# Kernel optimization log

Measured on AMD Instinct MI355X. Metric: run time of the kernel, lower is better.

Reference implementation:

```python
import jax, jax.numpy as jnp
import numpy as np

NUM_HEADS = 16
KEY_SIZE = 64
HEAD_SIZE = 64


def setup_inputs() -> dict:
    key = jax.random.key(0)
    ks = jax.random.split(key, 8)
    B, S, D = 2, 2048, 1024
    s = 1.0 / np.sqrt(D)
    return {
        "q": jax.random.normal(ks[0], (B, S, D), jnp.float32),
        "k": jax.random.normal(ks[1], (B, S, D), jnp.float32),
        "v": jax.random.normal(ks[2], (B, S, D), jnp.float32),
        "v_mask": jax.random.randint(ks[3], (B, S), 0, 2, jnp.int32),
        "Wq": jax.random.normal(ks[4], (D, NUM_HEADS * KEY_SIZE), jnp.float32) * s,
        "Wk": jax.random.normal(ks[5], (D, NUM_HEADS * KEY_SIZE), jnp.float32) * s,
        "Wv": jax.random.normal(ks[6], (D, NUM_HEADS * HEAD_SIZE), jnp.float32) * s,
    }


def reference(q, k, v, v_mask, Wq, Wk, Wv):
    B, Sq, _ = q.shape
    Sk = k.shape[1]
    # projections + split heads: [B, S, H, d]
    qw = (q @ Wq).reshape(B, Sq, NUM_HEADS, KEY_SIZE)
    kw = (k @ Wk).reshape(B, Sk, NUM_HEADS, KEY_SIZE)
    vw = (v @ Wv).reshape(B, Sk, NUM_HEADS, HEAD_SIZE)
    # scores [B, H, Sq, Sk]
    a = jnp.einsum('bqhd,bkhd->bhqk', qw, kw) / np.sqrt(KEY_SIZE).astype(np.float32)
    # additive mask over key axis: x*m - (1-m)*1e12
    m = v_mask.astype(a.dtype)[:, None, None, :]
    a = a * m - (1.0 - m) * 1e12
    a = jax.nn.softmax(a, axis=-1)
    # output [B, Sq, H*head_size]
    o = jnp.einsum('bhqk,bkhd->bqhd', a, vw)
    return o.reshape(B, Sq, NUM_HEADS * HEAD_SIZE)
```

## Files before the change

### kernel.cpp

```cpp
#include <hip/hip_runtime.h>
#include <hip/hip_bf16.h>


#define SEQ 2048
#define DIM 1024
#define NPROJ 1024

typedef __bf16 bf16x8 __attribute__((ext_vector_type(8)));
typedef float floatx4 __attribute__((ext_vector_type(4)));
typedef float floatx16 __attribute__((ext_vector_type(16)));

__device__ inline unsigned short f2bf_bits(float x) {
  __hip_bfloat16 h = __float2bfloat16(x);
  return __builtin_bit_cast(unsigned short, h);
}

__device__ __forceinline__ void gload_lds16(const void* g, void* l) {
  __builtin_amdgcn_global_load_lds((const __attribute__((address_space(1))) void*)g,
                                   (__attribute__((address_space(3))) void*)l, 16, 0, 0);
}

__global__ __launch_bounds__(256) void cvt_x(
    const float* __restrict__ q, const float* __restrict__ k, const float* __restrict__ v,
    unsigned short* __restrict__ xb)
{
  const float* X = blockIdx.z == 0 ? q : (blockIdx.z == 1 ? k : v);
  unsigned short* O = xb + (size_t)blockIdx.z * 4096 * 1024;
  int i0 = blockIdx.x * 256 + threadIdx.x;
  #pragma unroll
  for (int it = 0; it < 4; ++it) {
    int i = i0 + it * 262144;
    float4 f = *reinterpret_cast<const float4*>(&X[(size_t)i * 4]);
    ushort4 o;
    o.x = f2bf_bits(f.x); o.y = f2bf_bits(f.y);
    o.z = f2bf_bits(f.z); o.w = f2bf_bits(f.w);
    *reinterpret_cast<ushort4*>(&O[(size_t)i * 4]) = o;
  }
}

__global__ __launch_bounds__(256) void transpose_w(
    const float* __restrict__ Wq, const float* __restrict__ Wk, const float* __restrict__ Wv,
    unsigned short* __restrict__ WqT, unsigned short* __restrict__ WkT, unsigned short* __restrict__ WvT)
{
  const float* W = blockIdx.z == 0 ? Wq : (blockIdx.z == 1 ? Wk : Wv);
  unsigned short* WT = blockIdx.z == 0 ? WqT : (blockIdx.z == 1 ? WkT : WvT);
  const float sc = (blockIdx.z == 0) ? 0.1803368801f : 1.0f;
  __shared__ float tile[64][65];
  const int k0 = blockIdx.x * 64;
  const int n0 = blockIdx.y * 64;
  const int t = threadIdx.x;
  #pragma unroll
  for (int it = 0; it < 4; ++it) {
    int idx = t + (it << 8);
    int r = idx >> 4, c4 = (idx & 15) << 2;
    float4 v = *reinterpret_cast<const float4*>(&W[(k0 + r) * DIM + n0 + c4]);
    tile[r][c4 + 0] = v.x; tile[r][c4 + 1] = v.y;
    tile[r][c4 + 2] = v.z; tile[r][c4 + 3] = v.w;
  }
  __syncthreads();
  #pragma unroll
  for (int it = 0; it < 4; ++it) {
    int idx = t + (it << 8);
    int r = idx >> 4, c4 = (idx & 15) << 2;
    ushort4 o;
    o.x = f2bf_bits(tile[c4 + 0][r] * sc);
    o.y = f2bf_bits(tile[c4 + 1][r] * sc);
    o.z = f2bf_bits(tile[c4 + 2][r] * sc);
    o.w = f2bf_bits(tile[c4 + 3][r] * sc);
    *reinterpret_cast<ushort4*>(&WT[(n0 + r) * DIM + k0 + c4]) = o;
  }
}

__global__ __launch_bounds__(256, 4) void proj_gemm(
    const unsigned short* __restrict__ xb,
    const unsigned short* __restrict__ WqT, const unsigned short* __restrict__ WkT,
    const unsigned short* __restrict__ WvT,
    unsigned short* __restrict__ qw, unsigned short* __restrict__ kw, unsigned short* __restrict__ vw)
{
  const unsigned short* X = xb + (size_t)blockIdx.z * 4096 * 1024;
  const unsigned short* WT = blockIdx.z == 0 ? WqT : (blockIdx.z == 1 ? WkT : WvT);
  unsigned short* Y = blockIdx.z == 0 ? qw : (blockIdx.z == 1 ? kw : vw);

  __shared__ unsigned short Al[2][128 * 32];
  __shared__ unsigned short Bl[2][128 * 32];

  const int m0 = blockIdx.x * 128, n0 = blockIdx.y * 128;
  const int t = threadIdx.x;
  const int lane = t & 63;
  const int wid = t >> 6;
  const int wm = (wid >> 1) << 6, wn = (wid & 1) << 6;
  const int qd = lane >> 4, ln = lane & 15;

  auto stage = [&](int ks, int bi) {
    const int kb = ks << 6;
    #pragma unroll
    for (int i = 0; i < 2; ++i) {
      int p = t + (i << 8);
      int r = p >> 2, c = p & 3;
      int f = (r + (r >> 2)) & 3;
      gload_lds16((const char*)X + (size_t)(m0 + r) * 2048 + kb + ((c ^ f) << 4),
                  (char*)&Al[bi][0] + p * 16);
      gload_lds16((const char*)WT + (size_t)(n0 + r) * 2048 + kb + ((c ^ f) << 4),
                  (char*)&Bl[bi][0] + p * 16);
    }
  };

  floatx4 acc[4][4] = {};
  stage(0, 0);

  for (int ks = 0; ks < 32; ++ks) {
    __syncthreads();
    if (ks + 1 < 32) stage(ks + 1, (ks + 1) & 1);
    const int bi = ks & 1;
    bf16x8 af[4], bfr[4];
    #pragma unroll
    for (int mb = 0; mb < 4; ++mb) {
      int m = wm + mb * 16 + ln;
      int fm = (m + (m >> 2)) & 3;
      af[mb] = *reinterpret_cast<const bf16x8*>(&Al[bi][m * 32 + ((qd ^ fm) << 3)]);
    }
    #pragma unroll
    for (int nb = 0; nb < 4; ++nb) {
      int n = wn + nb * 16 + ln;
      int fn = (n + (n >> 2)) & 3;
      bfr[nb] = *reinterpret_cast<const bf16x8*>(&Bl[bi][n * 32 + ((qd ^ fn) << 3)]);
    }
    #pragma unroll
    for (int mb = 0; mb < 4; ++mb)
      #pragma unroll
      for (int nb = 0; nb < 4; ++nb)
        acc[mb][nb] = __builtin_amdgcn_mfma_f32_16x16x32_bf16(af[mb], bfr[nb], acc[mb][nb], 0, 0, 0);
  }
  #pragma unroll
  for (int mb = 0; mb < 4; ++mb)
    #pragma unroll
    for (int nb = 0; nb < 4; ++nb)
      #pragma unroll
      for (int i = 0; i < 4; ++i) {
        int m = m0 + wm + mb * 16 + qd * 4 + i;
        int n = n0 + wn + nb * 16 + ln;
        Y[(size_t)m * NPROJ + n] = f2bf_bits(acc[mb][nb][i]);
      }
}

__global__ __launch_bounds__(256) void transpose_v(
    const unsigned short* __restrict__ vw, const int* __restrict__ vmask,
    unsigned short* __restrict__ vt, unsigned short* __restrict__ mb)
{
  if (blockIdx.y == 0 && blockIdx.x < 16) {
    int i = blockIdx.x * 256 + threadIdx.x;
    mb[i] = vmask[i] ? 0x3F80 : 0;
  }
  __shared__ unsigned short tile[64 * 64];
  const int t = threadIdx.x;
  const int s0 = blockIdx.x * 64;
  const int bh = blockIdx.y;
  const int b = bh >> 4, h = bh & 15;
  #pragma unroll
  for (int it = 0; it < 2; ++it) {
    int p = t + (it << 8);
    int s = p >> 3, c = p & 7;
    int cp = (c + (s >> 3) + (s & 7)) & 7;
    int4 d = *reinterpret_cast<const int4*>(&vw[(size_t)(b * SEQ + s0 + s) * NPROJ + h * 64 + c * 8]);
    if (vmask[b * SEQ + s0 + s] == 0) { d.x = 0; d.y = 0; d.z = 0; d.w = 0; }
    *reinterpret_cast<int4*>(&tile[s * 64 + cp * 8]) = d;
  }
  __syncthreads();
  #pragma unroll
  for (int it = 0; it < 2; ++it) {
    int d = (t >> 3) + (it << 5), sc = t & 7;
    struct { alignas(16) unsigned short u[8]; } o;
    #pragma unroll
    for (int j = 0; j < 8; ++j) {
      int s = sc * 8 + j;
      int cp = ((d >> 3) + (s >> 3) + (s & 7)) & 7;
      o.u[j] = tile[s * 64 + cp * 8 + (d & 7)];
    }
    *reinterpret_cast<int4*>(&vt[(size_t)(bh * 64 + d) * SEQ + s0 + sc * 8]) =
        *reinterpret_cast<const int4*>(o.u);
  }
}

__global__ __launch_bounds__(256, 2) void attn_fwd(
    const unsigned short* __restrict__ qw, const unsigned short* __restrict__ kw,
    const unsigned short* __restrict__ vt, const unsigned short* __restrict__ mb,
    float* __restrict__ out)
{
  extern __shared__ char smem[];
  unsigned short* Kl = (unsigned short*)smem;
  unsigned short* Vl = (unsigned short*)(smem + 16384);
  unsigned short* Ml = (unsigned short*)(smem + 32768);

  const int t = threadIdx.x, lane = t & 63, wid = t >> 6;
  const int l5 = lane & 31, hi = lane >> 5;
  const int qh = wid >> 1, kh = wid & 1;
  const int bh = blockIdx.x;
  const int q0 = blockIdx.y * 128;
  const int b = bh >> 4, h = bh & 15;
  const int base = b * SEQ;

  auto stage = [&](int kt, int bi) {
    const int k0 = kt << 6;
    #pragma unroll
    for (int i = 0; i < 2; ++i) {
      int rb = wid * 16 + i * 8;
      int r = rb + (lane >> 3);
      int rsrc = (r & ~12) | ((r & 4) << 1) | ((r & 8) >> 1);
      int sw = ((lane & 7) ^ (r & 7)) << 4;
      gload_lds16((const char*)kw + ((size_t)((base + k0 + rsrc) * NPROJ + h * 64) << 1) + sw,
                  (char*)&Kl[bi * 4096] + rb * 128);
      gload_lds16((const char*)vt + ((size_t)((bh * 64 + r) * SEQ + k0) << 1) + sw,
                  (char*)&Vl[bi * 4096] + rb * 128);
    }
    if (wid == 3 && lane < 8)
      gload_lds16((const char*)mb + ((size_t)(base + k0 + lane * 8) << 1), (char*)&Ml[bi * 64]);
  };

  bf16x8 qfa[4], qfb[4];
  {
    const unsigned short* qpa =
        qw + (size_t)(base + q0 + qh * 64 + l5) * NPROJ + h * 64 + hi * 8;
    const unsigned short* qpb = qpa + (size_t)32 * NPROJ;
    #pragma unroll
    for (int kk = 0; kk < 4; ++kk) {
      qfa[kk] = *reinterpret_cast<const bf16x8*>(qpa + kk * 16);
      qfb[kk] = *reinterpret_cast<const bf16x8*>(qpb + kk * 16);
    }
  }

  floatx16 oa0a = {}, oa1a = {}, laa = {};
  floatx16 oa0b = {}, oa1b = {}, lab = {};
  stage(0, 0);

  #pragma unroll 2
  for (int kt = 0; kt < SEQ / 64; ++kt) {
    __syncthreads();
    if (kt + 1 < SEQ / 64) stage(kt + 1, (kt + 1) & 1);
    const int bi = kt & 1;

    floatx16 sa = {}, sb = {};
    __builtin_amdgcn_s_setprio(1);
    #pragma unroll
    for (int kk = 0; kk < 4; ++kk) {
      int ph = ((kk * 2 + hi) ^ (l5 & 7)) << 3;
      bf16x8 kf = *reinterpret_cast<const bf16x8*>(&Kl[bi * 4096 + (kh * 32 + l5) * 64 + ph]);
      sa = __builtin_amdgcn_mfma_f32_32x32x16_bf16(kf, qfa[kk], sa, 0, 0, 0);
      sb = __builtin_amdgcn_mfma_f32_32x32x16_bf16(kf, qfb[kk], sb, 0, 0, 0);
    }
    __builtin_amdgcn_s_setprio(0);

    float pea[16], peb[16];
    #pragma unroll
    for (int r = 0; r < 16; ++r) {
      pea[r] = __builtin_amdgcn_exp2f(sa[r]);
      peb[r] = __builtin_amdgcn_exp2f(sb[r]);
    }

    #pragma unroll
    for (int kk = 0; kk < 2; ++kk) {
      struct alignas(16) { unsigned short u[8]; } pka, pkb;
      #pragma unroll
      for (int j = 0; j < 8; ++j) {
        pka.u[j] = f2bf_bits(pea[8 * kk + j]);
        pkb.u[j] = f2bf_bits(peb[8 * kk + j]);
      }
      bf16x8 paa = __builtin_bit_cast(bf16x8, pka);
      bf16x8 pab = __builtin_bit_cast(bf16x8, pkb);
      int ch = ((4 * kh + 2 * kk + hi) ^ (l5 & 7)) << 3;
      bf16x8 v0 = *reinterpret_cast<const bf16x8*>(&Vl[bi * 4096 + l5 * 64 + ch]);
      bf16x8 v1 = *reinterpret_cast<const bf16x8*>(&Vl[bi * 4096 + (32 + l5) * 64 + ch]);
      bf16x8 mf = *reinterpret_cast<const bf16x8*>(&Ml[bi * 64 + kh * 32 + kk * 16 + hi * 8]);
      __builtin_amdgcn_s_setprio(1);
      oa0a = __builtin_amdgcn_mfma_f32_32x32x16_bf16(paa, v0, oa0a, 0, 0, 0);
      oa1a = __builtin_amdgcn_mfma_f32_32x32x16_bf16(paa, v1, oa1a, 0, 0, 0);
      laa  = __builtin_amdgcn_mfma_f32_32x32x16_bf16(paa, mf, laa, 0, 0, 0);
      oa0b = __builtin_amdgcn_mfma_f32_32x32x16_bf16(pab, v0, oa0b, 0, 0, 0);
      oa1b = __builtin_amdgcn_mfma_f32_32x32x16_bf16(pab, v1, oa1b, 0, 0, 0);
      lab  = __builtin_amdgcn_mfma_f32_32x32x16_bf16(pab, mf, lab, 0, 0, 0);
      __builtin_amdgcn_s_setprio(0);
    }
  }

  __syncthreads();
  float* Mg = (float*)smem;
  if (kh == 1) {
    #pragma unroll
    for (int r = 0; r < 16; ++r) {
      int m = (r & 3) + ((r >> 2) << 3) + (hi << 2);
      int rowa = qh * 64 + m, rowb = qh * 64 + 32 + m;
      Mg[rowa * 66 + l5] = oa0a[r];
      Mg[rowa * 66 + 32 + l5] = oa1a[r];
      Mg[rowb * 66 + l5] = oa0b[r];
      Mg[rowb * 66 + 32 + l5] = oa1b[r];
      if (l5 == 0) { Mg[rowa * 66 + 64] = laa[r]; Mg[rowb * 66 + 64] = lab[r]; }
    }
  }
  __syncthreads();
  if (kh == 0) {
    #pragma unroll
    for (int r = 0; r < 16; ++r) {
      int m = (r & 3) + ((r >> 2) << 3) + (hi << 2);
      int rowa = qh * 64 + m, rowb = qh * 64 + 32 + m;
      float o0a = oa0a[r] + Mg[rowa * 66 + l5];
      float o1a = oa1a[r] + Mg[rowa * 66 + 32 + l5];
      float inva = 1.0f / (laa[r] + Mg[rowa * 66 + 64]);
      size_t oa_ = (size_t)(base + q0 + rowa) * NPROJ + h * 64;
      out[oa_ + l5] = o0a * inva;
      out[oa_ + 32 + l5] = o1a * inva;
      float o0b = oa0b[r] + Mg[rowb * 66 + l5];
      float o1b = oa1b[r] + Mg[rowb * 66 + 32 + l5];
      float invb = 1.0f / (lab[r] + Mg[rowb * 66 + 64]);
      size_t ob_ = (size_t)(base + q0 + rowb) * NPROJ + h * 64;
      out[ob_ + l5] = o0b * invb;
      out[ob_ + 32 + l5] = o1b * invb;
    }
  }
}

extern "C" void kernel_launch(void* const* d_in, const int* in_sizes, int n_in,
                              void* d_out, int out_size, void* d_ws, size_t ws_size,
                              hipStream_t stream) {
  const float* q  = (const float*)d_in[0];
  const float* k  = (const float*)d_in[1];
  const float* v  = (const float*)d_in[2];
  const int* vm   = (const int*)d_in[3];
  const float* Wq = (const float*)d_in[4];
  const float* Wk = (const float*)d_in[5];
  const float* Wv = (const float*)d_in[6];
  float* out = (float*)d_out;

  unsigned short* ws = (unsigned short*)d_ws;
  unsigned short* WqT = ws + ((size_t)0 << 20);
  unsigned short* WkT = ws + ((size_t)1 << 20);
  unsigned short* WvT = ws + ((size_t)2 << 20);
  unsigned short* qw  = ws + ((size_t)3 << 20);
  unsigned short* kw  = ws + ((size_t)7 << 20);
  unsigned short* vw  = ws + ((size_t)11 << 20);
  unsigned short* xb  = ws + ((size_t)15 << 20);
  unsigned short* vt  = ws + ((size_t)15 << 20);
  unsigned short* mbv = WqT;

  cvt_x<<<dim3(1024, 1, 3), 256, 0, stream>>>(q, k, v, xb);
  transpose_w<<<dim3(16, 16, 3), 256, 0, stream>>>(Wq, Wk, Wv, WqT, WkT, WvT);
  proj_gemm<<<dim3(32, 8, 3), 256, 0, stream>>>(xb, WqT, WkT, WvT, qw, kw, vw);
  transpose_v<<<dim3(32, 32), 256, 0, stream>>>(vw, vm, vt, mbv);
  attn_fwd<<<dim3(32, 16), 256, 33792, stream>>>(qw, kw, vt, mbv, out);
}
```

Baseline: 102.9 us.

## Fuse fp32-to-bf16 input conversion into projection GEMM and enlarge attention blocks

Drops the separate cvt_x kernel: proj_gemm now reads fp32 activations directly into registers, converts them to bf16 and writes them to LDS, prefetching two K-steps ahead while weights still go through direct global-to-LDS loads. This removes a kernel launch and a full bf16 round trip of the activations through memory. Separately, attn_fwd moves to 512-thread blocks covering 256 query rows with twice the dynamic shared memory, so the K/V tiles are shared across more query rows. The fp32 loads are twice as wide as the old bf16 loads and go through registers, which adds register pressure. The attention hunk only partly shows the rest of the kernel, so it is unclear whether everything else was adapted to 8 waves.

```diff
diff --git a/kernel.cpp b/kernel.cpp
--- a/kernel.cpp
+++ b/kernel.cpp
@@ -18,24 +18,6 @@
 __device__ __forceinline__ void gload_lds16(const void* g, void* l) {
   __builtin_amdgcn_global_load_lds((const __attribute__((address_space(1))) void*)g,
                                    (__attribute__((address_space(3))) void*)l, 16, 0, 0);
-}
-
-__global__ __launch_bounds__(256) void cvt_x(
-    const float* __restrict__ q, const float* __restrict__ k, const float* __restrict__ v,
-    unsigned short* __restrict__ xb)
-{
-  const float* X = blockIdx.z == 0 ? q : (blockIdx.z == 1 ? k : v);
-  unsigned short* O = xb + (size_t)blockIdx.z * 4096 * 1024;
-  int i0 = blockIdx.x * 256 + threadIdx.x;
-  #pragma unroll
-  for (int it = 0; it < 4; ++it) {
-    int i = i0 + it * 262144;
-    float4 f = *reinterpret_cast<const float4*>(&X[(size_t)i * 4]);
-    ushort4 o;
-    o.x = f2bf_bits(f.x); o.y = f2bf_bits(f.y);
-    o.z = f2bf_bits(f.z); o.w = f2bf_bits(f.w);
-    *reinterpret_cast<ushort4*>(&O[(size_t)i * 4]) = o;
-  }
 }
 
 __global__ __launch_bounds__(256) void transpose_w(
@@ -72,12 +54,12 @@
 }
 
 __global__ __launch_bounds__(256, 4) void proj_gemm(
-    const unsigned short* __restrict__ xb,
+    const float* __restrict__ xq, const float* __restrict__ xk, const float* __restrict__ xv,
     const unsigned short* __restrict__ WqT, const unsigned short* __restrict__ WkT,
     const unsigned short* __restrict__ WvT,
     unsigned short* __restrict__ qw, unsigned short* __restrict__ kw, unsigned short* __restrict__ vw)
 {
-  const unsigned short* X = xb + (size_t)blockIdx.z * 4096 * 1024;
+  const float* X = blockIdx.z == 0 ? xq : (blockIdx.z == 1 ? xk : xv);
   const unsigned short* WT = blockIdx.z == 0 ? WqT : (blockIdx.z == 1 ? WkT : WvT);
   unsigned short* Y = blockIdx.z == 0 ? qw : (blockIdx.z == 1 ? kw : vw);
 
@@ -91,27 +73,58 @@
   const int wm = (wid >> 1) << 6, wn = (wid & 1) << 6;
   const int qd = lane >> 4, ln = lane & 15;
 
-  auto stage = [&](int ks, int bi) {
-    const int kb = ks << 6;
+  float4 ra[2], rb[2];
+
+  auto loadA = [&](int ks) {
     #pragma unroll
     for (int i = 0; i < 2; ++i) {
       int p = t + (i << 8);
       int r = p >> 2, c = p & 3;
       int f = (r + (r >> 2)) & 3;
-      gload_lds16((const char*)X + (size_t)(m0 + r) * 2048 + kb + ((c ^ f) << 4),
-                  (char*)&Al[bi][0] + p * 16);
-      gload_lds16((const char*)WT + (size_t)(n0 + r) * 2048 + kb + ((c ^ f) << 4),
+      const float* ga = X + (size_t)(m0 + r) * 1024 + ks * 32 + ((c ^ f) << 3);
+      ra[i] = *reinterpret_cast<const float4*>(ga);
+      rb[i] = *reinterpret_cast<const float4*>(ga + 4);
+    }
+  };
+  auto writeA = [&](int bi) {
+    #pragma unroll
+    for (int i = 0; i < 2; ++i) {
+      int p = t + (i << 8);
+      struct alignas(16) { unsigned short u[8]; } pk;
+      pk.u[0] = f2bf_bits(ra[i].x); pk.u[1] = f2bf_bits(ra[i].y);
+      pk.u[2] = f2bf_bits(ra[i].z); pk.u[3] = f2bf_bits(ra[i].w);
+      pk.u[4] = f2bf_bits(rb[i].x); pk.u[5] = f2bf_bits(rb[i].y);
+      pk.u[6] = f2bf_bits(rb[i].z); pk.u[7] = f2bf_bits(rb[i].w);
+      *reinterpret_cast<int4*>((char*)&Al[bi][0] + p * 16) =
+          *reinterpret_cast<const int4*>(pk.u);
+    }
+  };
+  auto loadB = [&](int ks, int bi) {
+    #pragma unroll
+    for (int i = 0; i < 2; ++i) {
+      int p = t + (i << 8);
+      int r = p >> 2, c = p & 3;
+      int f = (r + (r >> 2)) & 3;
+      gload_lds16((const char*)WT + (size_t)(n0 + r) * 2048 + (ks << 6) + ((c ^ f) << 4),
                   (char*)&Bl[bi][0] + p * 16);
     }
   };
 
   floatx4 acc[4][4] = {};
-  stage(0, 0);
+  loadB(0, 0);
+  loadA(0);
+  writeA(0);
+  loadA(1);
 
   for (int ks = 0; ks < 32; ++ks) {
     __syncthreads();
-    if (ks + 1 < 32) stage(ks + 1, (ks + 1) & 1);
     const int bi = ks & 1;
+    if (ks + 1 < 32) {
+      loadB(ks + 1, bi ^ 1);
+      writeA(bi ^ 1);
+    }
+    if (ks + 2 < 32) loadA(ks + 2);
+
     bf16x8 af[4], bfr[4];
     #pragma unroll
     for (int mb = 0; mb < 4; ++mb) {
@@ -181,7 +194,7 @@
   }
 }
 
-__global__ __launch_bounds__(256, 2) void attn_fwd(
+__global__ __launch_bounds__(512, 2) void attn_fwd(
     const unsigned short* __restrict__ qw, const unsigned short* __restrict__ kw,
     const unsigned short* __restrict__ vt, const unsigned short* __restrict__ mb,
     float* __restrict__ out)
@@ -195,24 +208,21 @@
   const int l5 = lane & 31, hi = lane >> 5;
   const int qh = wid >> 1, kh = wid & 1;
   const int bh = blockIdx.x;
-  const int q0 = blockIdx.y * 128;
+  const int q0 = blockIdx.y * 256;
   const int b = bh >> 4, h = bh & 15;
   const int base = b * SEQ;
 
   auto stage = [&](int kt, int bi) {
     const int k0 = kt << 6;
-    #pragma unroll
-    for (int i = 0; i < 2; ++i) {
-      int rb = wid * 16 + i * 8;
-      int r = rb + (lane >> 3);
-      int rsrc = (r & ~12) | ((r & 4) << 1) | ((r & 8) >> 1);
-      int sw = ((lane & 7) ^ (r & 7)) << 4;
-      gload_lds16((const char*)kw + ((size_t)((base + k0 + rsrc) * NPROJ + h * 64) << 1) + sw,
-                  (char*)&Kl[bi * 4096] + rb * 128);
-      gload_lds16((const char*)vt + ((size_t)((bh * 64 + r) * SEQ + k0) << 1) + sw,
-                  (char*)&Vl[bi * 4096] + rb * 128);
-    }
-    if (wid == 3 && lane < 8)
+    int rb = wid * 8;
+    int r = rb + (lane >> 3);
+    int rsrc = (r & ~12) | ((r & 4) << 1) | ((r & 8) >> 1);
+    int sw = ((lane & 7) ^ (r & 7)) << 4;
+    gload_lds16((const char*)kw + ((size_t)((base + k0 + rsrc) * NPROJ + h * 64) << 1) + sw,
+                (char*)&Kl[bi * 4096] + rb * 128);
+    gload_lds16((const char*)vt + ((size_t)((bh * 64 + r) * SEQ + k0) << 1) + sw,
+                (char*)&Vl[bi * 4096] + rb * 128);
+    if (wid == 7 && lane < 8)
       gload_lds16((const char*)mb + ((size_t)(base + k0 + lane * 8) << 1), (char*)&Ml[bi * 64]);
   };
 
@@ -336,13 +346,11 @@
   unsigned short* qw  = ws + ((size_t)3 << 20);
   unsigned short* kw  = ws + ((size_t)7 << 20);
   unsigned short* vw  = ws + ((size_t)11 << 20);
-  unsigned short* xb  = ws + ((size_t)15 << 20);
   unsigned short* vt  = ws + ((size_t)15 << 20);
   unsigned short* mbv = WqT;
 
-  cvt_x<<<dim3(1024, 1, 3), 256, 0, stream>>>(q, k, v, xb);
   transpose_w<<<dim3(16, 16, 3), 256, 0, stream>>>(Wq, Wk, Wv, WqT, WkT, WvT);
-  proj_gemm<<<dim3(32, 8, 3), 256, 0, stream>>>(xb, WqT, WkT, WvT, qw, kw, vw);
+  proj_gemm<<<dim3(32, 8, 3), 256, 0, stream>>>(q, k, v, WqT, WkT, WvT, qw, kw, vw);
   transpose_v<<<dim3(32, 32), 256, 0, stream>>>(vw, vm, vt, mbv);
-  attn_fwd<<<dim3(32, 16), 256, 33792, stream>>>(qw, kw, vt, mbv, out);
-}
+  attn_fwd<<<dim3(32, 8), 512, 67584, stream>>>(qw, kw, vt, mbv, out);
+}
```

Result: faster. 92.73 us (-9.9%).
